# Performance work log

Hardware: AMD Instinct MI355X
Metric: run time of the kernel (lower is better)

## Reference

```python
import jax, jax.numpy as jnp
import numpy as np

N = 8192   # nodes per graph
F = 128    # input feature dim
H = 512    # GAT hidden dim
D = 256    # GAT output dim (== match_size, required by matching broadcast)
MS = 256   # match_size
E = 131072 # edges per graph (one direction)
EPS = 1e-8 # torch cosine_similarity eps


def _xavier(k, shape):
    lim = (6.0 / (shape[0] + shape[-1])) ** 0.5
    return jax.random.uniform(k, shape, jnp.float32, -lim, lim)


def setup_inputs() -> dict:
    key = jax.random.key(0)
    ks = jax.random.split(key, 24)
    return {
        "x_s": jax.random.normal(ks[0], (N, F), jnp.float32),
        "x_t": jax.random.normal(ks[1], (N, F), jnp.float32),
        "edge_index_s": jax.random.randint(ks[2], (2, E), 0, N),
        "edge_index_t": jax.random.randint(ks[3], (2, E), 0, N),
        "label": jax.random.randint(ks[4], (1,), 0, 2),
        # GAT params (2 single-head layers)
        "W_g1": _xavier(ks[5], (F, H)),
        "a1_src": _xavier(ks[6], (H, 1))[:, 0],
        "a1_dst": _xavier(ks[7], (H, 1))[:, 0],
        "W_g2": _xavier(ks[8], (H, D)),
        "a2_src": _xavier(ks[9], (D, 1))[:, 0],
        "a2_dst": _xavier(ks[10], (D, 1))[:, 0],
        # readout_rep
        "W_read": _xavier(ks[11], (D, D)),
        # matching
        "W_match": _xavier(ks[12], (D, MS)),
        # MLP
        "mlp_w1": _xavier(ks[13], (MS * 8, MS * 2)), "mlp_b1": jnp.zeros((MS * 2,), jnp.float32),
        "mlp_w2": _xavier(ks[14], (MS * 2, MS)),     "mlp_b2": jnp.zeros((MS,), jnp.float32),
        "mlp_w3": _xavier(ks[15], (MS, MS // 2)),    "mlp_b3": jnp.zeros((MS // 2,), jnp.float32),
        "mlp_w4": _xavier(ks[16], (MS // 2, 1)),     "mlp_b4": jnp.zeros((1,), jnp.float32),
    }


def _gat_layer(h_in, src, dst, W, a_s, a_d, n):
    h = h_in @ W                                           # [n, d_out]
    logits = (h[src] * a_s).sum(-1) + (h[dst] * a_d).sum(-1)
    e = jax.nn.leaky_relu(logits, 0.2)
    m = jax.ops.segment_max(e, dst, num_segments=n)
    ex = jnp.exp(e - m[dst])
    den = jax.ops.segment_sum(ex, dst, num_segments=n)
    alpha = ex / (den[dst] + 1e-16)
    return jax.ops.segment_sum(alpha[:, None] * h[src], dst, num_segments=n)


def _gat(x, edge_index, W1, a1s, a1d, W2, a2s, a2d):
    n = x.shape[0]
    sl = jnp.arange(n)
    # symmetrize undirected edge list + add self loops (PyG GATConv convention)
    src = jnp.concatenate([edge_index[0], edge_index[1], sl])
    dst = jnp.concatenate([edge_index[1], edge_index[0], sl])
    h = jax.nn.elu(_gat_layer(x, src, dst, W1, a1s, a1d, n))
    return _gat_layer(h, src, dst, W2, a2s, a2d, n)


def _readout(h, W):
    g = jnp.tanh(jnp.mean(h, 0) @ W)                       # [d]
    s = jax.nn.sigmoid(h @ g)                              # [n]
    return (s[:, None] * h).sum(0, keepdims=True)          # [1, d]


def _match(h1, h2, Wm):
    # cosine over feature dim of (h * W) without materializing [N, D, MS]:
    # dot[n,m] = sum_d h1[n,d]*W[d,m]*h2[n,d]*W[d,m] = ((h1*h2) @ W^2)[n,m]
    W2 = Wm * Wm
    dot = (h1 * h2) @ W2
    n1 = jnp.sqrt((h1 * h1) @ W2)
    n2 = jnp.sqrt((h2 * h2) @ W2)
    return dot / jnp.maximum(n1 * n2, EPS)


def _mutual(h1, h2):
    n1 = jnp.linalg.norm(h1, axis=-1)
    n2 = jnp.linalg.norm(h2, axis=-1)
    cos = (h1 @ h2.T) / jnp.maximum(n1[:, None] * n2[None, :], EPS)  # [N, M]
    coe = cos / cos.sum(0)                                 # column-normalize
    return coe @ h2


def _mlp(z, w1, b1, w2, b2, w3, b3, w4, b4):
    z = jax.nn.relu(z @ w1 + b1)
    z = jax.nn.relu(z @ w2 + b2)
    z = jax.nn.relu(z @ w3 + b3)
    return jax.nn.sigmoid(z @ w4 + b4)


def _forward(x_s, x_t, edge_index_s, edge_index_t, label,
             W_g1, a1_src, a1_dst, W_g2, a2_src, a2_dst,
             W_read, W_match,
             mlp_w1, mlp_b1, mlp_w2, mlp_b2, mlp_w3, mlp_b3, mlp_w4, mlp_b4):
    f1 = (x_s - jnp.mean(x_s)) / jnp.std(x_s, ddof=1)
    f2 = (x_t - jnp.mean(x_t)) / jnp.std(x_t, ddof=1)

    h1 = _gat(f1, edge_index_s, W_g1, a1_src, a1_dst, W_g2, a2_src, a2_dst)
    h2 = _gat(f2, edge_index_t, W_g1, a1_src, a1_dst, W_g2, a2_src, a2_dst)

    h1g = _readout(h1, W_read)
    h2g = _readout(h2, W_read)

    h1m = _mutual(h1, h2)
    h2m = _mutual(h2, h1)
    h1mg = _readout(h1m, W_read)
    h2mg = _readout(h2m, W_read)

    miu1 = _match(h1, h1m, W_match); miu2 = _match(h2, h2m, W_match)
    miu1g = _readout(miu1, W_read);  miu2g = _readout(miu2, W_read)
    phi1 = _match(h1, h1mg, W_match); phi2 = _match(h2, h2mg, W_match)
    phi1g = _readout(phi1, W_read);   phi2g = _readout(phi2, W_read)
    psi1 = _match(h1g, h1m, W_match); psi2 = _match(h2g, h2m, W_match)
    psi1g = _readout(psi1, W_read);   psi2g = _readout(psi2, W_read)
    om1 = _match(h1g, h1mg, W_match); om2 = _match(h2g, h2mg, W_match)

    z1 = jnp.concatenate([miu1g, phi1g, psi1g, om1], axis=1).T  # [4*MS, 1]
    z2 = jnp.concatenate([miu2g, phi2g, psi2g, om2], axis=1).T
    z = jnp.concatenate([z1, z2], axis=0).T                     # [1, 8*MS]
    z = _mlp(z, mlp_w1, mlp_b1, mlp_w2, mlp_b2, mlp_w3, mlp_b3, mlp_w4, mlp_b4)
    return z


def reference(x_s, x_t, edge_index_s, edge_index_t, label,
              W_g1, a1_src, a1_dst, W_g2, a2_src, a2_dst,
              W_read, W_match,
              mlp_w1, mlp_b1, mlp_w2, mlp_b2, mlp_w3, mlp_b3, mlp_w4, mlp_b4):
    z = _forward(x_s, x_t, edge_index_s, edge_index_t, label,
                 W_g1, a1_src, a1_dst, W_g2, a2_src, a2_dst, W_read, W_match,
                 mlp_w1, mlp_b1, mlp_w2, mlp_b2, mlp_w3, mlp_b3, mlp_w4, mlp_b4)
    label_exp = jnp.exp(-label.astype(jnp.float32))
    return z, label, label_exp
```

## Files before the change

kernel.cpp:

```cpp
#include <hip/hip_runtime.h>
#include <hip/hip_bf16.h>
#include <math.h>
#include <stddef.h>

#define NN 8192
#define FF 128
#define HH 512
#define DDIM 256
#define EE 131072
#define ET (2*EE + NN)
#define FEPS 1e-8f

typedef float f32x4 __attribute__((ext_vector_type(4)));
typedef __bf16 bf16x8 __attribute__((ext_vector_type(8)));
typedef unsigned short u16;

static __device__ __forceinline__ u16 f2bf(float f) {
  union { float f; unsigned u; } v; v.f = f;
  return (u16)((v.u + 0x7fffu + ((v.u >> 16) & 1u)) >> 16);
}
static __device__ __forceinline__ float bf2f(u16 h) {
  union { unsigned u; float f; } v; v.u = ((unsigned)h) << 16;
  return v.f;
}
static __device__ __forceinline__ f32x4 mfma16(bf16x8 a, bf16x8 b, f32x4 c) {
  return __builtin_amdgcn_mfma_f32_16x16x32_bf16(a, b, c, 0, 0, 0);
}

struct PLF { const float* p[4]; };
struct PLB { const u16* p[6]; int slot[6]; };
struct MB6 { const float* X[6]; const float* Y[6]; int bx[6]; int by[6]; u16* o[6]; };

__global__ void k_reduce2(const float* __restrict__ xa, const float* __restrict__ xb,
                          int n, double* __restrict__ out) {
  const float* x = blockIdx.y ? xb : xa;
  double* o = out + 2 * blockIdx.y;
  __shared__ double s1[256], s2[256];
  double a = 0.0, b = 0.0;
  for (int i = blockIdx.x * blockDim.x + threadIdx.x; i < n; i += gridDim.x * blockDim.x) {
    double v = (double)x[i];
    a += v; b += v * v;
  }
  s1[threadIdx.x] = a; s2[threadIdx.x] = b;
  __syncthreads();
  for (int w = 128; w > 0; w >>= 1) {
    if (threadIdx.x < w) { s1[threadIdx.x] += s1[threadIdx.x + w]; s2[threadIdx.x] += s2[threadIdx.x + w]; }
    __syncthreads();
  }
  if (threadIdx.x == 0) { atomicAdd(&o[0], s1[0]); atomicAdd(&o[1], s2[0]); }
}

__global__ void k_normalize2(const float* __restrict__ xa, const float* __restrict__ xb,
                             u16* __restrict__ ya, u16* __restrict__ yb, int n,
                             const double* __restrict__ s) {
  const float* x = blockIdx.y ? xb : xa;
  u16* y = blockIdx.y ? yb : ya;
  const double* sp = s + 2 * blockIdx.y;
  double mean = sp[0] / (double)n;
  double var = (sp[1] - (double)n * mean * mean) / (double)(n - 1);
  float mu = (float)mean;
  float inv = (float)(1.0 / sqrt(var));
  for (int i = blockIdx.x * blockDim.x + threadIdx.x; i < n; i += gridDim.x * blockDim.x)
    y[i] = f2bf((x[i] - mu) * inv);
}

__global__ void k_hist(const int* __restrict__ ei, int* __restrict__ deg) {
  int t = blockIdx.x * blockDim.x + threadIdx.x;
  if (t >= ET) return;
  int dst = (t < EE) ? ei[EE + t] : ((t < 2*EE) ? ei[t - EE] : (t - 2*EE));
  atomicAdd(&deg[dst], 1);
}

__global__ void k_scan(const int* __restrict__ deg, int* __restrict__ offs, int* __restrict__ cursor) {
  __shared__ int ts[256];
  int tid = threadIdx.x;
  int loc[32];
  int s = 0;
  #pragma unroll
  for (int i = 0; i < 32; ++i) { loc[i] = s; s += deg[tid * 32 + i]; }
  ts[tid] = s;
  __syncthreads();
  for (int off = 1; off < 256; off <<= 1) {
    int v = (tid >= off) ? ts[tid - off] : 0;
    __syncthreads();
// ... 96 lines not shown
  if (as_) {
    float hsum[4] = {0.f, 0.f, 0.f, 0.f}, dsum[4] = {0.f, 0.f, 0.f, 0.f};
    #pragma unroll
    for (int n = 0; n < 8; ++n) {
      int c = n0 + n * 16 + r15;
      float av = as_[c], dv = ad_[c];
      #pragma unroll
      for (int q = 0; q < 4; ++q) { hsum[q] += acc[n][q] * av; dsum[q] += acc[n][q] * dv; }
    }
    #pragma unroll
    for (int q = 0; q < 4; ++q) {
      #pragma unroll
      for (int o = 1; o < 16; o <<= 1) { hsum[q] += __shfl_xor(hsum[q], o); dsum[q] += __shfl_xor(dsum[q], o); }
    }
    if (r15 == 0) {
      #pragma unroll
      for (int q = 0; q < 4; ++q) {
        atomicAdd(&hs[io + q], hsum[q]);
        atomicAdd(&hd[io + q], dsum[q]);
      }
    }
  }
}

__global__ void k_alpha(const int* __restrict__ offs, const int* __restrict__ srcs,
                        const float* __restrict__ hs, const float* __restrict__ hd,
                        float* __restrict__ alpha) {
  int wid = (blockIdx.x * blockDim.x + threadIdx.x) >> 6;
  int lane = threadIdx.x & 63;
  if (wid >= NN) return;
  int b = offs[wid], e = offs[wid + 1];
  float hdn = hd[wid];
  float m = -3.4e38f;
  for (int p = b + lane; p < e; p += 64) {
    float v = hs[srcs[p]] + hdn;
    v = v > 0.f ? v : 0.2f * v;
    alpha[p] = v;
    m = fmaxf(m, v);
  }
  #pragma unroll
  for (int o = 32; o > 0; o >>= 1) m = fmaxf(m, __shfl_xor(m, o));
  float den = 0.f;
  for (int p = b + lane; p < e; p += 64) {
    float ex = expf(alpha[p] - m);
    alpha[p] = ex;
    den += ex;
  }
  #pragma unroll
  for (int o = 32; o > 0; o >>= 1) den += __shfl_xor(den, o);
  float sc = 1.f / (den + 1e-16f);
  for (int p = b + lane; p < e; p += 64) alpha[p] *= sc;
}

__global__ __launch_bounds__(256) void k_agg2(const int* __restrict__ offs, const int* __restrict__ srcs,
                                              const float* __restrict__ alpha, const u16* __restrict__ Hb,
                                              float* __restrict__ outF, u16* __restrict__ outB,
                                              int D, int elu) {
  __shared__ float red[4][512];
  int n = blockIdx.x;
  int b = offs[n], e = offs[n + 1];
  int w = threadIdx.x >> 6, lane = threadIdx.x & 63;
  float acc[8];
  #pragma unroll
  for (int j = 0; j < 8; ++j) acc[j] = 0.f;
  if (D == 512) {
    const u16* base = Hb + lane * 8;
    for (int p = b + w; p < e; p += 4) {
      float a = alpha[p];
      uint4 v = *reinterpret_cast<const uint4*>(base + (size_t)srcs[p] * 512);
      acc[0] += a * bf2f((u16)(v.x & 0xffff)); acc[1] += a * bf2f((u16)(v.x >> 16));
      acc[2] += a * bf2f((u16)(v.y & 0xffff)); acc[3] += a * bf2f((u16)(v.y >> 16));
      acc[4] += a * bf2f((u16)(v.z & 0xffff)); acc[5] += a * bf2f((u16)(v.z >> 16));
      acc[6] += a * bf2f((u16)(v.w & 0xffff)); acc[7] += a * bf2f((u16)(v.w >> 16));
    }
    #pragma unroll
    for (int j = 0; j < 8; ++j) red[w][lane * 8 + j] = acc[j];
  } else {
    const u16* base = Hb + lane * 4;
    for (int p = b + w; p < e; p += 4) {
      float a = alpha[p];
      uint2 v = *reinterpret_cast<const uint2*>(base + (size_t)srcs[p] * 256);
      acc[0] += a * bf2f((u16)(v.x & 0xffff)); acc[1] += a * bf2f((u16)(v.x >> 16));
      acc[2] += a * bf2f((u16)(v.y & 0xffff)); acc[3] += a * bf2f((u16)(v.y >> 16));
    }
    #pragma unroll
    for (int j = 0; j < 4; ++j) red[w][lane * 4 + j] = acc[j];
  }
  __syncthreads();
  for (int dd = threadIdx.x; dd < D; dd += 256) {
    float sres = red[0][dd] + red[1][dd] + red[2][dd] + red[3][dd];
    if (elu) sres = sres > 0.f ? sres : (expf(sres) - 1.f);
    if (outF) outF[(size_t)n * D + dd] = sres;
    outB[(size_t)n * D + dd] = f2bf(sres);
  }
}

__global__ void k_rninv2(const float* __restrict__ h1, const float* __restrict__ h2,
                         float* __restrict__ o1, float* __restrict__ o2) {
  const float* h = blockIdx.y ? h2 : h1;
  float* o = blockIdx.y ? o2 : o1;
  int wid = (blockIdx.x * blockDim.x + threadIdx.x) >> 6;
  int lane = threadIdx.x & 63;
  if (wid >= NN) return;
  float4 v = *reinterpret_cast<const float4*>(h + (size_t)wid * DDIM + lane * 4);
  float a = v.x * v.x + v.y * v.y + v.z * v.z + v.w * v.w;
  #pragma unroll
  for (int o2_ = 32; o2_ > 0; o2_ >>= 1) a += __shfl_xor(a, o2_);
  if (!lane) o[wid] = 1.f / sqrtf(a);
}

__global__ void k_wsum(const float* __restrict__ h1, const float* __restrict__ h2,
                       const float* __restrict__ n1inv, const float* __restrict__ n2inv,
                       float* __restrict__ ut) {
  const float* h = blockIdx.y ? h2 : h1;
  const float* wv = blockIdx.y ? n2inv : n1inv;
  float* o = ut + 256 * blockIdx.y;
  int d = threadIdx.x;
  int r0 = blockIdx.x * 128;
  float acc = 0.f;
  for (int r = 0; r < 128; ++r) acc += wv[r0 + r] * h[(size_t)(r0 + r) * 256 + d];
  atomicAdd(&o[d], acc);
}

__global__ void k_rs(const float* __restrict__ h1, const float* __restrict__ h2,
                     const float* __restrict__ n1inv, const float* __restrict__ n2inv,
                     const float* __restrict__ ut, float* __restrict__ R, float* __restrict__ S) {
  const float* h  = blockIdx.y ? h2 : h1;
  const float* ni = blockIdx.y ? n2inv : n1inv;
  const float* gv = blockIdx.y ? ut : ut + 256;
  float* o = blockIdx.y ? S : R;
  int wid = (blockIdx.x * blockDim.x + threadIdx.x) >> 6;
  int lane = threadIdx.x & 63;
  if (wid >= NN) return;
  float4 v = *reinterpret_cast<const float4*>(h + (size_t)wid * 256 + lane * 4);
  float4 g4 = *reinterpret_cast<const float4*>(gv + lane * 4);
  float a = v.x * g4.x + v.y * g4.y + v.z * g4.z + v.w * g4.w;
  #pragma unroll
  for (int o2_ = 32; o2_ > 0; o2_ >>= 1) a += __shfl_xor(a, o2_);
  if (!lane) o[wid] = ni[wid] * a;
}

__global__ void k_scj(const float* __restrict__ S, const float* __restrict__ R,
                      const float* __restrict__ n1inv, const float* __restrict__ n2inv,
                      float* __restrict__ scj1, float* __restrict__ scj2) {
  int j = blockIdx.x * blockDim.x + threadIdx.x;
  if (j >= NN) return;
  scj1[j] = n2inv[j] / S[j];
  scj2[j] = n1inv[j] / R[j];
}

__global__ __launch_bounds__(256) void k_gemm_M(const u16* __restrict__ A1, const u16* __restrict__ B1,
                                                const u16* __restrict__ A2, const u16* __restrict__ B2,
                                                float* __restrict__ Mf) {
  int mat = blockIdx.z & 1, kch = blockIdx.z >> 1;
  const u16* A = mat ? A2 : A1;
  const u16* Bt = mat ? B2 : B1;
  float* C = Mf + mat * 65536;
  int w = threadIdx.x >> 6, l = threadIdx.x & 63, r15 = l & 15, g = l >> 4;
  int i0 = blockIdx.y * 64 + w * 16;
  int n0 = blockIdx.x * 128;
  f32x4 zero = {0.f, 0.f, 0.f, 0.f};
  f32x4 acc[8];
  #pragma unroll
  for (int n = 0; n < 8; ++n) acc[n] = zero;
  const u16* arow = A + (size_t)(i0 + r15) * NN + g * 8;
  for (int kc = kch * 16; kc < kch * 16 + 16; ++kc) {
    bf16x8 a = *reinterpret_cast<const bf16x8*>(arow + kc * 32);
    #pragma unroll
    for (int n = 0; n < 8; ++n) {
      bf16x8 b = *reinterpret_cast<const bf16x8*>(Bt + (size_t)(n0 + n * 16 + r15) * NN + kc * 32 + g * 8);
      acc[n] = mfma16(a, b, acc[n]);
    }
  }
  int io = i0 + g * 4;
  #pragma unroll
  for (int n = 0; n < 8; ++n) {
    int c = n0 + n * 16 + r15;
    #pragma unroll
    for (int q = 0; q < 4; ++q)
      atomicAdd(&C[(size_t)(io + q) * 256 + c], acc[n][q]);
  }
}

__global__ void k_m2bf(const float* __restrict__ Mf, u16* __restrict__ Mb) {
  size_t o = (size_t)blockIdx.y * 65536 + blockIdx.x * 256 + threadIdx.x;
  Mb[o] = f2bf(Mf[o]);
}

__global__ __launch_bounds__(256) void k_gemm_hm(const u16* __restrict__ A1, const u16* __restrict__ M1,
                                                 const float* __restrict__ s1, float* __restrict__ O1,
                                                 const u16* __restrict__ A2, const u16* __restrict__ M2,
                                                 const float* __restrict__ s2, float* __restrict__ O2) {
  int z = blockIdx.z;
  const u16* A = z ? A2 : A1;
  const u16* Bt = z ? M2 : M1;
  const float* sc = z ? s2 : s1;
  float* O = z ? O2 : O1;
  int w = threadIdx.x >> 6, l = threadIdx.x & 63, r15 = l & 15, g = l >> 4;
  int i0 = blockIdx.y * 64 + w * 16;
  int n0 = blockIdx.x * 128;
  f32x4 zero = {0.f, 0.f, 0.f, 0.f};
  f32x4 acc[8];
  #pragma unroll
  for (int n = 0; n < 8; ++n) acc[n] = zero;
  const u16* arow = A + (size_t)(i0 + r15) * 256 + g * 8;
  #pragma unroll
  for (int kc = 0; kc < 8; ++kc) {
    bf16x8 a = *reinterpret_cast<const bf16x8*>(arow + kc * 32);
    #pragma unroll
    for (int n = 0; n < 8; ++n) {
      bf16x8 b = *reinterpret_cast<const bf16x8*>(Bt + (size_t)(n0 + n * 16 + r15) * 256 + kc * 32 + g * 8);
      acc[n] = mfma16(a, b, acc[n]);
    }
  }
  int io = i0 + g * 4;
  float s4[4];
  #pragma unroll
  for (int q = 0; q < 4; ++q) s4[q] = sc[io + q];
  #pragma unroll
  for (int n = 0; n < 8; ++n) {
    int c = n0 + n * 16 + r15;
    #pragma unroll
    for (int q = 0; q < 4; ++q)
      O[(size_t)(io + q) * 256 + c] = acc[n][q] * s4[q];
  }
}

__global__ __launch_bounds__(256) void k_match_b6(MB6 M, const u16* __restrict__ W2t) {
  int z = blockIdx.z;
  const float* X = M.X[z];
  const float* Y = M.Y[z];
  int bx = M.bx[z], by = M.by[z];
  u16* outb = M.o[z];
  int w = threadIdx.x >> 6, l = threadIdx.x & 63, r15 = l & 15, g = l >> 4;
  int i0 = blockIdx.y * 64 + w * 16;
  int n0 = blockIdx.x * 128;
  f32x4 zero = {0.f, 0.f, 0.f, 0.f};
  f32x4 aU[8], aP[8], aQ[8];
  #pragma unroll
  for (int n = 0; n < 8; ++n) { aU[n] = zero; aP[n] = zero; aQ[n] = zero; }
  int row = i0 + r15;
  const float* xr = X + (size_t)(bx ? 0 : row) * 256;
  const float* yr = Y + (size_t)(by ? 0 : row) * 256;
  #pragma unroll 2
  for (int kc = 0; kc < 8; ++kc) {
    int base = kc * 32 + g * 8;
    float4 x0 = *reinterpret_cast<const float4*>(xr + base);
    float4 x1 = *reinterpret_cast<const float4*>(xr + base + 4);
    float4 y0 = *reinterpret_cast<const float4*>(yr + base);
    float4 y1 = *reinterpret_cast<const float4*>(yr + base + 4);
    bf16x8 fu, fp, fq;
    fu[0] = (__bf16)(x0.x * y0.x); fu[1] = (__bf16)(x0.y * y0.y);
    fu[2] = (__bf16)(x0.z * y0.z); fu[3] = (__bf16)(x0.w * y0.w);
    fu[4] = (__bf16)(x1.x * y1.x); fu[5] = (__bf16)(x1.y * y1.y);
    fu[6] = (__bf16)(x1.z * y1.z); fu[7] = (__bf16)(x1.w * y1.w);
    fp[0] = (__bf16)(x0.x * x0.x); fp[1] = (__bf16)(x0.y * x0.y);
    fp[2] = (__bf16)(x0.z * x0.z); fp[3] = (__bf16)(x0.w * x0.w);
    fp[4] = (__bf16)(x1.x * x1.x); fp[5] = (__bf16)(x1.y * x1.y);
    fp[6] = (__bf16)(x1.z * x1.z); fp[7] = (__bf16)(x1.w * x1.w);
    fq[0] = (__bf16)(y0.x * y0.x); fq[1] = (__bf16)(y0.y * y0.y);
    fq[2] = (__bf16)(y0.z * y0.z); fq[3] = (__bf16)(y0.w * y0.w);
    fq[4] = (__bf16)(y1.x * y1.x); fq[5] = (__bf16)(y1.y * y1.y);
    fq[6] = (__bf16)(y1.z * y1.z); fq[7] = (__bf16)(y1.w * y1.w);
    #pragma unroll
    for (int n = 0; n < 8; ++n) {
      bf16x8 b = *reinterpret_cast<const bf16x8*>(W2t + (size_t)(n0 + n * 16 + r15) * 256 + kc * 32 + g * 8);
      aU[n] = mfma16(fu, b, aU[n]);
      aP[n] = mfma16(fp, b, aP[n]);
      aQ[n] = mfma16(fq, b, aQ[n]);
    }
  }
  int io = i0 + g * 4;
  #pragma unroll
  for (int n = 0; n < 8; ++n) {
    int c = n0 + n * 16 + r15;
    #pragma unroll
    for (int q = 0; q < 4; ++q) {
      float s = sqrtf(aP[n][q]) * sqrtf(aQ[n][q]);
      outb[(size_t)(io + q) * 256 + c] = f2bf(aU[n][q] / fmaxf(s, FEPS));
    }
  }
}

__global__ void k_match_g(const float* __restrict__ X1, const float* __restrict__ Y1,
                          const float* __restrict__ X2, const float* __restrict__ Y2,
                          const float* __restrict__ W2, float* __restrict__ v) {
  __shared__ float u[256], p[256], q[256];
  const float* X = blockIdx.x ? X2 : X1;
  const float* Y = blockIdx.x ? Y2 : Y1;
  float* o = v + (blockIdx.x ? 1792 : 768);
  int t = threadIdx.x;
  float xv = X[t], yv = Y[t];
  u[t] = xv * yv; p[t] = xv * xv; q[t] = yv * yv;
  __syncthreads();
  float a = 0.f, b = 0.f, c = 0.f;
  #pragma unroll 4
  for (int d = 0; d < 256; ++d) {
    float wv = W2[(size_t)d * DDIM + t];
    a += u[d] * wv; b += p[d] * wv; c += q[d] * wv;
  }
  o[t] = a / fmaxf(sqrtf(b) * sqrtf(c), FEPS);
}

__global__ void k_w2(const float* __restrict__ Wm, float* __restrict__ W2, int n) {
  int i = blockIdx.x * blockDim.x + threadIdx.x;
  if (i < n) { float v = Wm[i]; W2[i] = v * v; }
}

__global__ void k_bmu_f(PLF L, float* __restrict__ mu) {
  const float* h = L.p[blockIdx.y];
  int d = threadIdx.x;
  int r0 = blockIdx.x * 128;
  float acc = 0.f;
  for (int r = 0; r < 128; ++r) acc += h[(size_t)(r0 + r) * 256 + d];
  atomicAdd(&mu[blockIdx.y * 256 + d], acc);
}

__global__ void k_bmu_b(PLB L, float* __restrict__ mu) {
  const u16* h = L.p[blockIdx.y];
  int d = threadIdx.x;
  int r0 = blockIdx.x * 128;
  float acc = 0.f;
  for (int r = 0; r < 128; ++r) acc += bf2f(h[(size_t)(r0 + r) * 256 + d]);
  atomicAdd(&mu[blockIdx.y * 256 + d], acc);
}

__global__ void k_bgv(const float* __restrict__ mu, const float* __restrict__ Wr,
                      float* __restrict__ g) {
  __shared__ float ls[256];
  int m = blockIdx.x, t = threadIdx.x;
  ls[t] = mu[m * 256 + t] * (1.f / (float)NN);
  __syncthreads();
  float acc = 0.f;
  #pragma unroll 4
  for (int d = 0; d < 256; ++d) acc += ls[d] * Wr[(size_t)d * 256 + t];
  g[m * 256 + t] = tanhf(acc);
}

__global__ __launch_bounds__(256) void k_bsc_f(PLF L, const float* __restrict__ g,
                                               float* __restrict__ ogbase) {
  __shared__ __align__(16) float gs[256];
  __shared__ float sarr[32];
  int m = blockIdx.y;
  const float* h = L.p[m];
  int t = threadIdx.x, w = t >> 6, l = t & 63;
  gs[t] = g[m * 256 + t];
  __syncthreads();
  int r0 = blockIdx.x * 32;
  float4 gv4 = reinterpret_cast<const float4*>(gs)[l];
  for (int rr = w * 8; rr < w * 8 + 8; ++rr) {
    float4 hv = reinterpret_cast<const float4*>(h + (size_t)(r0 + rr) * 256)[l];
    float dot = hv.x * gv4.x + hv.y * gv4.y + hv.z * gv4.z + hv.w * gv4.w;
    #pragma unroll
    for (int o = 32; o > 0; o >>= 1) dot += __shfl_xor(dot, o);
    if (!l) sarr[rr] = 1.f / (1.f + expf(-dot));
  }
  __syncthreads();
  float acc = 0.f;
  for (int rr = 0; rr < 32; ++rr) acc += sarr[rr] * h[(size_t)(r0 + rr) * 256 + t];
  atomicAdd(&ogbase[m * 256 + t], acc);
}

__global__ __launch_bounds__(256) void k_bsc_b(PLB L, const float* __restrict__ g,
                                               float* __restrict__ v) {
  __shared__ __align__(16) float gs[256];
  __shared__ float sarr[32];
  int m = blockIdx.y;
  const u16* h = L.p[m];
  int t = threadIdx.x, w = t >> 6, l = t & 63;
  gs[t] = g[m * 256 + t];
  __syncthreads();
  int r0 = blockIdx.x * 32;
  float4 gv4 = reinterpret_cast<const float4*>(gs)[l];
  for (int rr = w * 8; rr < w * 8 + 8; ++rr) {
    ushort4 hv = *reinterpret_cast<const ushort4*>(h + (size_t)(r0 + rr) * 256 + l * 4);
    float dot = bf2f(hv.x) * gv4.x + bf2f(hv.y) * gv4.y + bf2f(hv.z) * gv4.z + bf2f(hv.w) * gv4.w;
    #pragma unroll
    for (int o = 32; o > 0; o >>= 1) dot += __shfl_xor(dot, o);
    if (!l) sarr[rr] = 1.f / (1.f + expf(-dot));
  }
  __syncthreads();
  float acc = 0.f;
  for (int rr = 0; rr < 32; ++rr) acc += sarr[rr] * bf2f(h[(size_t)(r0 + rr) * 256 + t]);
  atomicAdd(&v[L.slot[m] + t], acc);
}

__global__ void k_binit(const float* __restrict__ b1, const float* __restrict__ b2,
                        const float* __restrict__ b3, float* __restrict__ l1,
                        float* __restrict__ l2, float* __restrict__ l3) {
  int t = blockIdx.x * 256 + threadIdx.x;
  if (t < 512) l1[t] = b1[t];
  if (t < 256) l2[t] = b2[t];
  if (t < 128) l3[t] = b3[t];
}

__global__ void k_gemv(const float* __restrict__ vin, const float* __restrict__ w,
                       float* __restrict__ out, int K, int M, int Kc, int relu_in) {
  int m = blockIdx.x * 256 + threadIdx.x;
  if (m >= M) return;
  int k0 = blockIdx.y * Kc;
  float acc = 0.f;
  #pragma unroll 4
  for (int k = k0; k < k0 + Kc; ++k) {
    float x = vin[k];
    if (relu_in) x = fmaxf(x, 0.f);
    acc += x * w[(size_t)k * M + m];
  }
  atomicAdd(&out[m], acc);
}

__global__ void k_final(const float* __restrict__ l3, const float* __restrict__ w4,
                        const float* __restrict__ b4, const int* __restrict__ label,
                        float* __restrict__ out) {
  __shared__ float ls[128];
  int t = threadIdx.x;
  ls[t] = fmaxf(l3[t], 0.f) * w4[t];
  __syncthreads();
  for (int w = 64; w > 0; w >>= 1) { if (t < w) ls[t] += ls[t + w]; __syncthreads(); }
  if (t == 0) {
    float z = 1.f / (1.f + expf(-(ls[0] + b4[0])));
    out[0] = z;
    float lb = (float)label[0];
    out[1] = lb;
    out[2] = expf(-lb);
  }
}

extern "C" void kernel_launch(void* const* d_in, const int* in_sizes, int n_in,
                              void* d_out, int out_size, void* d_ws, size_t ws_size,
                              hipStream_t stream) {
  (void)in_sizes; (void)n_in; (void)out_size;
  const float* x_s   = (const float*)d_in[0];
  const float* x_t   = (const float*)d_in[1];
  const int*   ei_s  = (const int*)d_in[2];
  const int*   ei_t  = (const int*)d_in[3];
  const int*   label = (const int*)d_in[4];
  const float* W_g1  = (const float*)d_in[5];
  const float* a1s   = (const float*)d_in[6];
  const float* a1d   = (const float*)d_in[7];
  const float* W_g2  = (const float*)d_in[8];
  const float* a2s   = (const float*)d_in[9];
  const float* a2d   = (const float*)d_in[10];
  const float* W_read  = (const float*)d_in[11];
  const float* W_match = (const float*)d_in[12];
  const float* w1 = (const float*)d_in[13]; const float* b1 = (const float*)d_in[14];
  const float* w2 = (const float*)d_in[15]; const float* b2 = (const float*)d_in[16];
  const float* w3 = (const float*)d_in[17]; const float* b3 = (const float*)d_in[18];
  const float* w4 = (const float*)d_in[19]; const float* b4 = (const float*)d_in[20];
  float* out = (float*)d_out;

  char* base = (char*)d_ws;
  size_t off = 0;
  auto alloc = [&](size_t bytes) -> void* {
    void* pp = base + off;
    off = (off + bytes + 255) & ~(size_t)255;
    return pp;
  };
  double* dsum = (double*)alloc(4 * sizeof(double));
  u16*   hb_bf= (u16*)alloc((size_t)NN * HH * 2);
  u16*   aggb = (u16*)alloc((size_t)NN * HH * 2);
  float* h1   = (float*)alloc((size_t)NN * DDIM * 4);
  float* h2   = (float*)alloc((size_t)NN * DDIM * 4);
  float* h1m  = (float*)alloc((size_t)NN * DDIM * 4);
  float* h2m  = (float*)alloc((size_t)NN * DDIM * 4);
  u16*   f1b  = (u16*)alloc((size_t)NN * FF * 2);
  u16*   f2b  = (u16*)alloc((size_t)NN * FF * 2);
  u16*   h1b  = (u16*)alloc((size_t)NN * DDIM * 2);
  u16*   h2b  = (u16*)alloc((size_t)NN * DDIM * 2);
  u16*   h1t  = (u16*)alloc((size_t)NN * DDIM * 2);
  u16*   h2t  = (u16*)alloc((size_t)NN * DDIM * 2);
  u16*   wh1t = (u16*)alloc((size_t)NN * DDIM * 2);
  u16*   wh2t = (u16*)alloc((size_t)NN * DDIM * 2);
  u16*   mb0  = (u16*)alloc((size_t)NN * DDIM * 2);
  u16*   mb1  = (u16*)alloc((size_t)NN * DDIM * 2);
  u16*   mb2  = (u16*)alloc((size_t)NN * DDIM * 2);
  u16*   mb3  = (u16*)alloc((size_t)NN * DDIM * 2);
  u16*   mb4  = (u16*)alloc((size_t)NN * DDIM * 2);
  u16*   mb5  = (u16*)alloc((size_t)NN * DDIM * 2);
  float* alpha= (float*)alloc((size_t)ET * 4);
  int*   srcs = (int*)alloc((size_t)ET * 4);
  int*   deg  = (int*)alloc(NN * 4);
  int*   curs = (int*)alloc(NN * 4);
  int*   offs = (int*)alloc((NN + 1) * 4);
  float* n1inv= (float*)alloc(NN * 4);
  float* n2inv= (float*)alloc(NN * 4);
  float* Rr   = (float*)alloc(NN * 4);
  float* Ss   = (float*)alloc(NN * 4);
  float* scj1 = (float*)alloc(NN * 4);
  float* scj2 = (float*)alloc(NN * 4);
  float* hsb  = (float*)alloc(NN * 4);
  float* hdb  = (float*)alloc(NN * 4);
  float* W2   = (float*)alloc((size_t)DDIM * DDIM * 4);
  u16*   Wg1t = (u16*)alloc((size_t)HH * FF * 2);
  u16*   Wg2t = (u16*)alloc((size_t)DDIM * HH * 2);
  u16*   W2t  = (u16*)alloc((size_t)DDIM * DDIM * 2);
  u16*   Mb   = (u16*)alloc(2 * 65536 * 2);
  float* mug1 = (float*)alloc(4 * 256 * 4);
  float* ogs  = (float*)alloc(4 * 256 * 4);
  float* mug2 = (float*)alloc(6 * 256 * 4);
  float* v    = (float*)alloc(2048 * 4);
  float* ut   = (float*)alloc(512 * 4);
  float* Mf   = (float*)alloc(2 * 65536 * 4);
  float* g1   = (float*)alloc(4 * 256 * 4);
  float* g2   = (float*)alloc(6 * 256 * 4);
  float* l1o  = (float*)alloc(512 * 4);
  float* l2o  = (float*)alloc(256 * 4);
  float* l3o  = (float*)alloc(128 * 4);
  if (off > ws_size) return;

  float* h1g  = ogs + 0;
  float* h2g  = ogs + 256;
  float* h1mg = ogs + 512;
  float* h2mg = ogs + 768;
  const size_t zr_bytes = (4 * 256 + 4 * 256 + 6 * 256 + 2048 + 512 + 2 * 65536) * 4;

  hipMemsetAsync(dsum, 0, 4 * sizeof(double), stream);
  k_reduce2<<<dim3(1024, 2), 256, 0, stream>>>(x_s, x_t, NN * FF, dsum);
  k_normalize2<<<dim3(1024, 2), 256, 0, stream>>>(x_s, x_t, f1b, f2b, NN * FF, dsum);

  k_tr_bf16<<<dim3(HH / 32, FF / 32), 256, 0, stream>>>(W_g1, Wg1t, FF, HH, 0);
  k_tr_bf16<<<dim3(DDIM / 32, HH / 32), 256, 0, stream>>>(W_g2, Wg2t, HH, DDIM, 0);
  k_tr_bf16<<<dim3(DDIM / 32, DDIM / 32), 256, 0, stream>>>(W_match, W2t, DDIM, DDIM, 1);
  k_w2<<<dim3((DDIM * DDIM + 255) / 256), 256, 0, stream>>>(W_match, W2, DDIM * DDIM);

  auto run_gat = [&](const u16* finb, const int* ei, float* hout, u16* houtb) {
    hipMemsetAsync(deg, 0, NN * 4, stream);
    k_hist<<<dim3((ET + 255) / 256), 256, 0, stream>>>(ei, deg);
    k_scan<<<1, 256, 0, stream>>>(deg, offs, curs);
    k_scatter<<<dim3((ET + 255) / 256), 256, 0, stream>>>(ei, curs, srcs);
    hipMemsetAsync(hsb, 0, 2 * NN * 4, stream);
    k_gemm_bf<<<dim3(HH / 128, NN / 64), 256, 0, stream>>>(finb, Wg1t, hb_bf, FF, HH, a1s, a1d, hsb, hdb);
    k_alpha<<<dim3(NN / 4), 256, 0, stream>>>(offs, srcs, hsb, hdb, alpha);
    k_agg2<<<dim3(NN), 256, 0, stream>>>(offs, srcs, alpha, hb_bf, nullptr, aggb, HH, 1);
    hipMemsetAsync(hsb, 0, 2 * NN * 4, stream);
    k_gemm_bf<<<dim3(DDIM / 128, NN / 64), 256, 0, stream>>>(aggb, Wg2t, hb_bf, HH, DDIM, a2s, a2d, hsb, hdb);
    k_alpha<<<dim3(NN / 4), 256, 0, stream>>>(offs, srcs, hsb, hdb, alpha);
    k_agg2<<<dim3(NN), 256, 0, stream>>>(offs, srcs, alpha, hb_bf, hout, houtb, DDIM, 0);
  };
  run_gat(f1b, ei_s, h1, h1b);
  run_gat(f2b, ei_t, h2, h2b);

  k_rninv2<<<dim3(NN / 4, 2), 256, 0, stream>>>(h1, h2, n1inv, n2inv);
  hipMemsetAsync(mug1, 0, zr_bytes, stream);
  k_wsum<<<dim3(64, 2), 256, 0, stream>>>(h1, h2, n1inv, n2inv, ut);
  k_rs<<<dim3(NN / 4, 2), 256, 0, stream>>>(h1, h2, n1inv, n2inv, ut, Rr, Ss);
  k_scj<<<dim3(NN / 256), 256, 0, stream>>>(Ss, Rr, n1inv, n2inv, scj1, scj2);
  k_tr2w<<<dim3(DDIM / 32, NN / 32, 2), 256, 0, stream>>>(h2, scj1, h2t, wh2t, h1, scj2, h1t, wh1t);
  k_gemm_M<<<dim3(2, 4, 32), 256, 0, stream>>>(wh2t, h2t, wh1t, h1t, Mf);
  k_m2bf<<<dim3(256, 2), 256, 0, stream>>>(Mf, Mb);
  k_gemm_hm<<<dim3(2, 128, 2), 256, 0, stream>>>(h1b, Mb, n1inv, h1m,
                                                 h2b, Mb + 65536, n2inv, h2m);

  PLF g1l; g1l.p[0] = h1; g1l.p[1] = h2; g1l.p[2] = h1m; g1l.p[3] = h2m;
  k_bmu_f<<<dim3(64, 4), 256, 0, stream>>>(g1l, mug1);
  k_bgv<<<dim3(4), 256, 0, stream>>>(mug1, W_read, g1);
  k_bsc_f<<<dim3(256, 4), 256, 0, stream>>>(g1l, g1, ogs);

  MB6 m6;
  m6.X[0] = h1;  m6.Y[0] = h1m;  m6.bx[0] = 0; m6.by[0] = 0; m6.o[0] = mb0;
  m6.X[1] = h1;  m6.Y[1] = h1mg; m6.bx[1] = 0; m6.by[1] = 1; m6.o[1] = mb1;
  m6.X[2] = h1g; m6.Y[2] = h1m;  m6.bx[2] = 1; m6.by[2] = 0; m6.o[2] = mb2;
  m6.X[3] = h2;  m6.Y[3] = h2m;  m6.bx[3] = 0; m6.by[3] = 0; m6.o[3] = mb3;
  m6.X[4] = h2;  m6.Y[4] = h2mg; m6.bx[4] = 0; m6.by[4] = 1; m6.o[4] = mb4;
  m6.X[5] = h2g; m6.Y[5] = h2m;  m6.bx[5] = 1; m6.by[5] = 0; m6.o[5] = mb5;
  k_match_b6<<<dim3(2, NN / 64, 6), 256, 0, stream>>>(m6, W2t);
  k_match_g<<<dim3(2), 256, 0, stream>>>(h1g, h1mg, h2g, h2mg, W2, v);

  PLB g2l;
  g2l.p[0] = mb0; g2l.slot[0] = 0;
  g2l.p[1] = mb1; g2l.slot[1] = 256;
  g2l.p[2] = mb2; g2l.slot[2] = 512;
  g2l.p[3] = mb3; g2l.slot[3] = 1024;
  g2l.p[4] = mb4; g2l.slot[4] = 1280;
  g2l.p[5] = mb5; g2l.slot[5] = 1536;
  k_bmu_b<<<dim3(64, 6), 256, 0, stream>>>(g2l, mug2);
  k_bgv<<<dim3(6), 256, 0, stream>>>(mug2, W_read, g2);
  k_bsc_b<<<dim3(256, 6), 256, 0, stream>>>(g2l, g2, v);

  k_binit<<<dim3(2), 256, 0, stream>>>(b1, b2, b3, l1o, l2o, l3o);
  k_gemv<<<dim3(2, 16), 256, 0, stream>>>(v, w1, l1o, 2048, 512, 128, 0);
  k_gemv<<<dim3(1, 8), 256, 0, stream>>>(l1o, w2, l2o, 512, 256, 64, 1);
  k_gemv<<<dim3(1, 8), 256, 0, stream>>>(l2o, w3, l3o, 256, 128, 32, 1);
  k_final<<<1, 128, 0, stream>>>(l3o, w4, b4, label, out);
}
```

Baseline: 711.7 us.

## Factor matching norms into precomputed reciprocals, bf16 intermediates, per-wave aggregation

The fused matching kernel, which ran three MFMA accumulations (product, x-norm and y-norm) for each of six pairs, is restructured. Squared-norm GEMMs are now computed once per feature matrix into reciprocal-root tables. Broadcast-vector cases fold the global vector into a pre-scaled weight matrix, so each of the six pairs needs only one GEMM. The matched features h1m/h2m are stored in bf16, and the readout kernels now read bf16 instead of fp32. GAT aggregation is changed to one wave per node with no shared-memory reduction. Together these cut MFMA work and memory traffic, at the cost of extra precision loss from storing the reciprocal norms in bf16.

```diff
diff --git a/kernel.cpp b/kernel.cpp
--- a/kernel.cpp
+++ b/kernel.cpp
@@ -27,9 +27,11 @@
   return __builtin_amdgcn_mfma_f32_16x16x32_bf16(a, b, c, 0, 0, 0);
 }
 
-struct PLF { const float* p[4]; };
 struct PLB { const u16* p[6]; int slot[6]; };
-struct MB6 { const float* X[6]; const float* Y[6]; int bx[6]; int by[6]; u16* o[6]; };
+struct MM {
+  const u16* A1[6]; const u16* A2[6]; const u16* B[6];
+  const u16* R1[6]; const u16* R2[6]; const float* Y[6]; u16* o[6];
+};
 
 __global__ void k_reduce2(const float* __restrict__ xa, const float* __restrict__ xb,
                           int n, double* __restrict__ out) {
@@ -232,20 +234,19 @@
   for (int p = b + lane; p < e; p += 64) alpha[p] *= sc;
 }
 
-__global__ __launch_bounds__(256) void k_agg2(const int* __restrict__ offs, const int* __restrict__ srcs,
+__global__ __launch_bounds__(256) void k_agg3(const int* __restrict__ offs, const int* __restrict__ srcs,
                                               const float* __restrict__ alpha, const u16* __restrict__ Hb,
                                               float* __restrict__ outF, u16* __restrict__ outB,
                                               int D, int elu) {
-  __shared__ float red[4][512];
-  int n = blockIdx.x;
+  int wv = threadIdx.x >> 6, lane = threadIdx.x & 63;
+  int n = blockIdx.x * 4 + wv;
   int b = offs[n], e = offs[n + 1];
-  int w = threadIdx.x >> 6, lane = threadIdx.x & 63;
-  float acc[8];
-  #pragma unroll
-  for (int j = 0; j < 8; ++j) acc[j] = 0.f;
   if (D == 512) {
+    float acc[8];
+    #pragma unroll
+    for (int j = 0; j < 8; ++j) acc[j] = 0.f;
     const u16* base = Hb + lane * 8;
-    for (int p = b + w; p < e; p += 4) {
+    for (int p = b; p < e; ++p) {
       float a = alpha[p];
       uint4 v = *reinterpret_cast<const uint4*>(base + (size_t)srcs[p] * 512);
       acc[0] += a * bf2f((u16)(v.x & 0xffff)); acc[1] += a * bf2f((u16)(v.x >> 16));
@@ -253,25 +254,36 @@
       acc[4] += a * bf2f((u16)(v.z & 0xffff)); acc[5] += a * bf2f((u16)(v.z >> 16));
       acc[6] += a * bf2f((u16)(v.w & 0xffff)); acc[7] += a * bf2f((u16)(v.w >> 16));
     }
-    #pragma unroll
-    for (int j = 0; j < 8; ++j) red[w][lane * 8 + j] = acc[j];
+    ushort4 o0, o1;
+    #pragma unroll
+    for (int j = 0; j < 8; ++j)
+      if (elu) acc[j] = acc[j] > 0.f ? acc[j] : (expf(acc[j]) - 1.f);
+    o0.x = f2bf(acc[0]); o0.y = f2bf(acc[1]); o0.z = f2bf(acc[2]); o0.w = f2bf(acc[3]);
+    o1.x = f2bf(acc[4]); o1.y = f2bf(acc[5]); o1.z = f2bf(acc[6]); o1.w = f2bf(acc[7]);
+    u16* ob = outB + (size_t)n * 512 + lane * 8;
+    *reinterpret_cast<ushort4*>(ob) = o0;
+    *reinterpret_cast<ushort4*>(ob + 4) = o1;
   } else {
+    float acc[4];
+    #pragma unroll
+    for (int j = 0; j < 4; ++j) acc[j] = 0.f;
     const u16* base = Hb + lane * 4;
-    for (int p = b + w; p < e; p += 4) {
+    for (int p = b; p < e; ++p) {
       float a = alpha[p];
       uint2 v = *reinterpret_cast<const uint2*>(base + (size_t)srcs[p] * 256);
       acc[0] += a * bf2f((u16)(v.x & 0xffff)); acc[1] += a * bf2f((u16)(v.x >> 16));
       acc[2] += a * bf2f((u16)(v.y & 0xffff)); acc[3] += a * bf2f((u16)(v.y >> 16));
     }
     #pragma unroll
-    for (int j = 0; j < 4; ++j) red[w][lane * 4 + j] = acc[j];
-  }
-  __syncthreads();
-  for (int dd = threadIdx.x; dd < D; dd += 256) {
-    float sres = red[0][dd] + red[1][dd] + red[2][dd] + red[3][dd];
-    if (elu) sres = sres > 0.f ? sres : (expf(sres) - 1.f);
-    if (outF) outF[(size_t)n * D + dd] = sres;
-    outB[(size_t)n * D + dd] = f2bf(sres);
+    for (int j = 0; j < 4; ++j)
+      if (elu) acc[j] = acc[j] > 0.f ? acc[j] : (expf(acc[j]) - 1.f);
+    if (outF) {
+      float4 of = {acc[0], acc[1], acc[2], acc[3]};
+      *reinterpret_cast<float4*>(outF + (size_t)n * 256 + lane * 4) = of;
+    }
+    ushort4 ob;
+    ob.x = f2bf(acc[0]); ob.y = f2bf(acc[1]); ob.z = f2bf(acc[2]); ob.w = f2bf(acc[3]);
+    *reinterpret_cast<ushort4*>(outB + (size_t)n * 256 + lane * 4) = ob;
   }
 }
 
@@ -368,14 +380,14 @@
 }
 
 __global__ __launch_bounds__(256) void k_gemm_hm(const u16* __restrict__ A1, const u16* __restrict__ M1,
-                                                 const float* __restrict__ s1, float* __restrict__ O1,
+                                                 const float* __restrict__ s1, u16* __restrict__ O1,
                                                  const u16* __restrict__ A2, const u16* __restrict__ M2,
-                                                 const float* __restrict__ s2, float* __restrict__ O2) {
+                                                 const float* __restrict__ s2, u16* __restrict__ O2) {
   int z = blockIdx.z;
   const u16* A = z ? A2 : A1;
   const u16* Bt = z ? M2 : M1;
   const float* sc = z ? s2 : s1;
-  float* O = z ? O2 : O1;
+  u16* O = z ? O2 : O1;
   int w = threadIdx.x >> 6, l = threadIdx.x & 63, r15 = l & 15, g = l >> 4;
   int i0 = blockIdx.y * 64 + w * 16;
   int n0 = blockIdx.x * 128;
@@ -402,62 +414,124 @@
     int c = n0 + n * 16 + r15;
     #pragma unroll
     for (int q = 0; q < 4; ++q)
-      O[(size_t)(io + q) * 256 + c] = acc[n][q] * s4[q];
-  }
-}
-
-__global__ __launch_bounds__(256) void k_match_b6(MB6 M, const u16* __restrict__ W2t) {
+      O[(size_t)(io + q) * 256 + c] = f2bf(acc[n][q] * s4[q]);
+  }
+}
+
+__global__ __launch_bounds__(256) void k_matchA(const u16* __restrict__ A0, const u16* __restrict__ A1,
+                                                const u16* __restrict__ A2_, const u16* __restrict__ A3,
+                                                const u16* __restrict__ W2t,
+                                                u16* __restrict__ r0, u16* __restrict__ r1,
+                                                u16* __restrict__ r2, u16* __restrict__ r3) {
   int z = blockIdx.z;
-  const float* X = M.X[z];
+  const u16* A = z == 0 ? A0 : z == 1 ? A1 : z == 2 ? A2_ : A3;
+  u16* outR = z == 0 ? r0 : z == 1 ? r1 : z == 2 ? r2 : r3;
+  int w = threadIdx.x >> 6, l = threadIdx.x & 63, r15 = l & 15, g = l >> 4;
+  int i0 = blockIdx.y * 64 + w * 16;
+  int n0 = blockIdx.x * 128;
+  f32x4 zero = {0.f, 0.f, 0.f, 0.f};
+  f32x4 acc[8];
+  #pragma unroll
+  for (int n = 0; n < 8; ++n) acc[n] = zero;
+  const u16* arow = A + (size_t)(i0 + r15) * 256 + g * 8;
+  #pragma unroll
+  for (int kc = 0; kc < 8; ++kc) {
+    uint4 xv = *reinterpret_cast<const uint4*>(arow + kc * 32);
+    bf16x8 fp;
+    float t;
+    t = bf2f((u16)(xv.x & 0xffff)); fp[0] = (__bf16)(t * t);
+    t = bf2f((u16)(xv.x >> 16));    fp[1] = (__bf16)(t * t);
+    t = bf2f((u16)(xv.y & 0xffff)); fp[2] = (__bf16)(t * t);
+    t = bf2f((u16)(xv.y >> 16));    fp[3] = (__bf16)(t * t);
+    t = bf2f((u16)(xv.z & 0xffff)); fp[4] = (__bf16)(t * t);
+    t = bf2f((u16)(xv.z >> 16));    fp[5] = (__bf16)(t * t);
+    t = bf2f((u16)(xv.w & 0xffff)); fp[6] = (__bf16)(t * t);
+    t = bf2f((u16)(xv.w >> 16));    fp[7] = (__bf16)(t * t);
+    #pragma unroll
+    for (int n = 0; n < 8; ++n) {
+      bf16x8 b = *reinterpret_cast<const bf16x8*>(W2t + (size_t)(n0 + n * 16 + r15) * 256 + kc * 32 + g * 8);
+      acc[n] = mfma16(fp, b, acc[n]);
+    }
+  }
+  int io = i0 + g * 4;
+  #pragma unroll
+  for (int n = 0; n < 8; ++n) {
+    int c = n0 + n * 16 + r15;
+    #pragma unroll
+    for (int q = 0; q < 4; ++q)
+      outR[(size_t)(io + q) * 256 + c] = f2bf(rsqrtf(fmaxf(acc[n][q], 1e-30f)));
+  }
+}
+
+__global__ void k_w2d(const u16* __restrict__ W2t, const float* __restrict__ ogs,
+                      u16* __restrict__ W2d, float* __restrict__ yn) {
+  __shared__ float red[256];
+  int n = blockIdx.x, z = blockIdx.y, k = threadIdx.x;
+  int map = (z == 0) ? 512 : (z == 1) ? 0 : (z == 2) ? 768 : 256;
+  float y = ogs[map + k];
+  float wv = bf2f(W2t[n * 256 + k]);
+  W2d[z * 65536 + n * 256 + k] = f2bf(wv * y);
+  red[k] = wv * y * y;
+  __syncthreads();
+  for (int s = 128; s > 0; s >>= 1) {
+    if (k < s) red[k] += red[k + s];
+    __syncthreads();
+  }
+  if (!k) yn[z * 256 + n] = rsqrtf(fmaxf(red[0], 1e-30f));
+}
+
+__global__ __launch_bounds__(256) void k_matchB(MM M) {
+  int z = blockIdx.z;
+  const u16* A1 = M.A1[z];
+  const u16* A2 = M.A2[z];
+  const u16* Bt = M.B[z];
+  const u16* R1 = M.R1[z];
+  const u16* R2 = M.R2[z];
   const float* Y = M.Y[z];
-  int bx = M.bx[z], by = M.by[z];
   u16* outb = M.o[z];
   int w = threadIdx.x >> 6, l = threadIdx.x & 63, r15 = l & 15, g = l >> 4;
   int i0 = blockIdx.y * 64 + w * 16;
   int n0 = blockIdx.x * 128;
   f32x4 zero = {0.f, 0.f, 0.f, 0.f};
-  f32x4 aU[8], aP[8], aQ[8];
-  #pragma unroll
-  for (int n = 0; n < 8; ++n) { aU[n] = zero; aP[n] = zero; aQ[n] = zero; }
-  int row = i0 + r15;
-  const float* xr = X + (size_t)(bx ? 0 : row) * 256;
-  const float* yr = Y + (size_t)(by ? 0 : row) * 256;
-  #pragma unroll 2
+  f32x4 acc[8];
+  #pragma unroll
+  for (int n = 0; n < 8; ++n) acc[n] = zero;
+  size_t abase = (size_t)(i0 + r15) * 256 + g * 8;
+  #pragma unroll
   for (int kc = 0; kc < 8; ++kc) {
-    int base = kc * 32 + g * 8;
-    float4 x0 = *reinterpret_cast<const float4*>(xr + base);
-    float4 x1 = *reinterpret_cast<const float4*>(xr + base + 4);
-    float4 y0 = *reinterpret_cast<const float4*>(yr + base);
-    float4 y1 = *reinterpret_cast<const float4*>(yr + base + 4);
-    bf16x8 fu, fp, fq;
-    fu[0] = (__bf16)(x0.x * y0.x); fu[1] = (__bf16)(x0.y * y0.y);
-    fu[2] = (__bf16)(x0.z * y0.z); fu[3] = (__bf16)(x0.w * y0.w);
-    fu[4] = (__bf16)(x1.x * y1.x); fu[5] = (__bf16)(x1.y * y1.y);
-    fu[6] = (__bf16)(x1.z * y1.z); fu[7] = (__bf16)(x1.w * y1.w);
-    fp[0] = (__bf16)(x0.x * x0.x); fp[1] = (__bf16)(x0.y * x0.y);
-    fp[2] = (__bf16)(x0.z * x0.z); fp[3] = (__bf16)(x0.w * x0.w);
-    fp[4] = (__bf16)(x1.x * x1.x); fp[5] = (__bf16)(x1.y * x1.y);
-    fp[6] = (__bf16)(x1.z * x1.z); fp[7] = (__bf16)(x1.w * x1.w);
-    fq[0] = (__bf16)(y0.x * y0.x); fq[1] = (__bf16)(y0.y * y0.y);
-    fq[2] = (__bf16)(y0.z * y0.z); fq[3] = (__bf16)(y0.w * y0.w);
-    fq[4] = (__bf16)(y1.x * y1.x); fq[5] = (__bf16)(y1.y * y1.y);
-    fq[6] = (__bf16)(y1.z * y1.z); fq[7] = (__bf16)(y1.w * y1.w);
+    bf16x8 fa;
+    uint4 a = *reinterpret_cast<const uint4*>(A1 + abase + kc * 32);
+    if (A2) {
+      uint4 b2 = *reinterpret_cast<const uint4*>(A2 + abase + kc * 32);
+      fa[0] = (__bf16)(bf2f((u16)(a.x & 0xffff)) * bf2f((u16)(b2.x & 0xffff)));
+      fa[1] = (__bf16)(bf2f((u16)(a.x >> 16))    * bf2f((u16)(b2.x >> 16)));
+      fa[2] = (__bf16)(bf2f((u16)(a.y & 0xffff)) * bf2f((u16)(b2.y & 0xffff)));
+      fa[3] = (__bf16)(bf2f((u16)(a.y >> 16))    * bf2f((u16)(b2.y >> 16)));
+      fa[4] = (__bf16)(bf2f((u16)(a.z & 0xffff)) * bf2f((u16)(b2.z & 0xffff)));
+      fa[5] = (__bf16)(bf2f((u16)(a.z >> 16))    * bf2f((u16)(b2.z >> 16)));
+      fa[6] = (__bf16)(bf2f((u16)(a.w & 0xffff)) * bf2f((u16)(b2.w & 0xffff)));
+      fa[7] = (__bf16)(bf2f((u16)(a.w >> 16))    * bf2f((u16)(b2.w >> 16)));
+    } else {
+      fa = *reinterpret_cast<const bf16x8*>(&a);
+    }
     #pragma unroll
     for (int n = 0; n < 8; ++n) {
-      bf16x8 b = *reinterpret_cast<const bf16x8*>(W2t + (size_t)(n0 + n * 16 + r15) * 256 + kc * 32 + g * 8);
-      aU[n] = mfma16(fu, b, aU[n]);
-      aP[n] = mfma16(fp, b, aP[n]);
-      aQ[n] = mfma16(fq, b, aQ[n]);
+      bf16x8 b = *reinterpret_cast<const bf16x8*>(Bt + (size_t)(n0 + n * 16 + r15) * 256 + kc * 32 + g * 8);
+      acc[n] = mfma16(fa, b, acc[n]);
     }
   }
   int io = i0 + g * 4;
   #pragma unroll
   for (int n = 0; n < 8; ++n) {
     int c = n0 + n * 16 + r15;
+    float yc = Y ? Y[c] : 1.f;
     #pragma unroll
     for (int q = 0; q < 4; ++q) {
-      float s = sqrtf(aP[n][q]) * sqrtf(aQ[n][q]);
-      outb[(size_t)(io + q) * 256 + c] = f2bf(aU[n][q] / fmaxf(s, FEPS));
+      float sc = yc;
+      size_t idx = (size_t)(io + q) * 256 + c;
+      if (R1) sc *= bf2f(R1[idx]);
+      if (R2) sc *= bf2f(R2[idx]);
+      outb[idx] = f2bf(acc[n][q] * sc);
     }
   }
 }
@@ -487,15 +561,6 @@
   if (i < n) { float v = Wm[i]; W2[i] = v * v; }
 }
 
-__global__ void k_bmu_f(PLF L, float* __restrict__ mu) {
-  const float* h = L.p[blockIdx.y];
-  int d = threadIdx.x;
-  int r0 = blockIdx.x * 128;
-  float acc = 0.f;
-  for (int r = 0; r < 128; ++r) acc += h[(size_t)(r0 + r) * 256 + d];
-  atomicAdd(&mu[blockIdx.y * 256 + d], acc);
-}
-
 __global__ void k_bmu_b(PLB L, float* __restrict__ mu) {
   const u16* h = L.p[blockIdx.y];
   int d = threadIdx.x;
@@ -515,30 +580,6 @@
   #pragma unroll 4
   for (int d = 0; d < 256; ++d) acc += ls[d] * Wr[(size_t)d * 256 + t];
   g[m * 256 + t] = tanhf(acc);
-}
-
-__global__ __launch_bounds__(256) void k_bsc_f(PLF L, const float* __restrict__ g,
-                                               float* __restrict__ ogbase) {
-  __shared__ __align__(16) float gs[256];
-  __shared__ float sarr[32];
-  int m = blockIdx.y;
-  const float* h = L.p[m];
-  int t = threadIdx.x, w = t >> 6, l = t & 63;
-  gs[t] = g[m * 256 + t];
-  __syncthreads();
-  int r0 = blockIdx.x * 32;
-  float4 gv4 = reinterpret_cast<const float4*>(gs)[l];
-  for (int rr = w * 8; rr < w * 8 + 8; ++rr) {
-    float4 hv = reinterpret_cast<const float4*>(h + (size_t)(r0 + rr) * 256)[l];
-    float dot = hv.x * gv4.x + hv.y * gv4.y + hv.z * gv4.z + hv.w * gv4.w;
-    #pragma unroll
-    for (int o = 32; o > 0; o >>= 1) dot += __shfl_xor(dot, o);
-    if (!l) sarr[rr] = 1.f / (1.f + expf(-dot));
-  }
-  __syncthreads();
-  float acc = 0.f;
-  for (int rr = 0; rr < 32; ++rr) acc += sarr[rr] * h[(size_t)(r0 + rr) * 256 + t];
-  atomicAdd(&ogbase[m * 256 + t], acc);
 }
 
 __global__ __launch_bounds__(256) void k_bsc_b(PLB L, const float* __restrict__ g,
@@ -641,12 +682,12 @@
   u16*   aggb = (u16*)alloc((size_t)NN * HH * 2);
   float* h1   = (float*)alloc((size_t)NN * DDIM * 4);
   float* h2   = (float*)alloc((size_t)NN * DDIM * 4);
-  float* h1m  = (float*)alloc((size_t)NN * DDIM * 4);
-  float* h2m  = (float*)alloc((size_t)NN * DDIM * 4);
   u16*   f1b  = (u16*)alloc((size_t)NN * FF * 2);
   u16*   f2b  = (u16*)alloc((size_t)NN * FF * 2);
   u16*   h1b  = (u16*)alloc((size_t)NN * DDIM * 2);
   u16*   h2b  = (u16*)alloc((size_t)NN * DDIM * 2);
+  u16*   h1mb = (u16*)alloc((size_t)NN * DDIM * 2);
+  u16*   h2mb = (u16*)alloc((size_t)NN * DDIM * 2);
   u16*   h1t  = (u16*)alloc((size_t)NN * DDIM * 2);
   u16*   h2t  = (u16*)alloc((size_t)NN * DDIM * 2);
   u16*   wh1t = (u16*)alloc((size_t)NN * DDIM * 2);
@@ -657,6 +698,10 @@
   u16*   mb3  = (u16*)alloc((size_t)NN * DDIM * 2);
   u16*   mb4  = (u16*)alloc((size_t)NN * DDIM * 2);
   u16*   mb5  = (u16*)alloc((size_t)NN * DDIM * 2);
+  u16*   rP1  = (u16*)alloc((size_t)NN * DDIM * 2);
+  u16*   rQ1  = (u16*)alloc((size_t)NN * DDIM * 2);
+  u16*   rP2  = (u16*)alloc((size_t)NN * DDIM * 2);
+  u16*   rQ2  = (u16*)alloc((size_t)NN * DDIM * 2);
   float* alpha= (float*)alloc((size_t)ET * 4);
   int*   srcs = (int*)alloc((size_t)ET * 4);
   int*   deg  = (int*)alloc(NN * 4);
@@ -674,6 +719,8 @@
   u16*   Wg1t = (u16*)alloc((size_t)HH * FF * 2);
   u16*   Wg2t = (u16*)alloc((size_t)DDIM * HH * 2);
   u16*   W2t  = (u16*)alloc((size_t)DDIM * DDIM * 2);
+  u16*   W2dB = (u16*)alloc(4 * 65536 * 2);
+  float* ynB  = (float*)alloc(4 * 256 * 4);
   u16*   Mb   = (u16*)alloc(2 * 65536 * 2);
   float* mug1 = (float*)alloc(4 * 256 * 4);
   float* ogs  = (float*)alloc(4 * 256 * 4);
@@ -711,11 +758,11 @@
     hipMemsetAsync(hsb, 0, 2 * NN * 4, stream);
     k_gemm_bf<<<dim3(HH / 128, NN / 64), 256, 0, stream>>>(finb, Wg1t, hb_bf, FF, HH, a1s, a1d, hsb, hdb);
     k_alpha<<<dim3(NN / 4), 256, 0, stream>>>(offs, srcs, hsb, hdb, alpha);
-    k_agg2<<<dim3(NN), 256, 0, stream>>>(offs, srcs, alpha, hb_bf, nullptr, aggb, HH, 1);
+    k_agg3<<<dim3(NN / 4), 256, 0, stream>>>(offs, srcs, alpha, hb_bf, nullptr, aggb, HH, 1);
     hipMemsetAsync(hsb, 0, 2 * NN * 4, stream);
     k_gemm_bf<<<dim3(DDIM / 128, NN / 64), 256, 0, stream>>>(aggb, Wg2t, hb_bf, HH, DDIM, a2s, a2d, hsb, hdb);
     k_alpha<<<dim3(NN / 4), 256, 0, stream>>>(offs, srcs, hsb, hdb, alpha);
-    k_agg2<<<dim3(NN), 256, 0, stream>>>(offs, srcs, alpha, hb_bf, hout, houtb, DDIM, 0);
+    k_agg3<<<dim3(NN / 4), 256, 0, stream>>>(offs, srcs, alpha, hb_bf, hout, houtb, DDIM, 0);
   };
   run_gat(f1b, ei_s, h1, h1b);
   run_gat(f2b, ei_t, h2, h2b);
@@ -728,22 +775,29 @@
   k_tr2w<<<dim3(DDIM / 32, NN / 32, 2), 256, 0, stream>>>(h2, scj1, h2t, wh2t, h1, scj2, h1t, wh1t);
   k_gemm_M<<<dim3(2, 4, 32), 256, 0, stream>>>(wh2t, h2t, wh1t, h1t, Mf);
   k_m2bf<<<dim3(256, 2), 256, 0, stream>>>(Mf, Mb);
-  k_gemm_hm<<<dim3(2, 128, 2), 256, 0, stream>>>(h1b, Mb, n1inv, h1m,
-                                                 h2b, Mb + 65536, n2inv, h2m);
-
-  PLF g1l; g1l.p[0] = h1; g1l.p[1] = h2; g1l.p[2] = h1m; g1l.p[3] = h2m;
-  k_bmu_f<<<dim3(64, 4), 256, 0, stream>>>(g1l, mug1);
+  k_gemm_hm<<<dim3(2, 128, 2), 256, 0, stream>>>(h1b, Mb, n1inv, h1mb,
+                                                 h2b, Mb + 65536, n2inv, h2mb);
+
+  k_matchA<<<dim3(2, 128, 4), 256, 0, stream>>>(h1b, h1mb, h2b, h2mb, W2t, rP1, rQ1, rP2, rQ2);
+
+  PLB g1l;
+  g1l.p[0] = h1b;  g1l.slot[0] = 0;
+  g1l.p[1] = h2b;  g1l.slot[1] = 256;
+  g1l.p[2] = h1mb; g1l.slot[2] = 512;
+  g1l.p[3] = h2mb; g1l.slot[3] = 768;
+  k_bmu_b<<<dim3(64, 4), 256, 0, stream>>>(g1l, mug1);
   k_bgv<<<dim3(4), 256, 0, stream>>>(mug1, W_read, g1);
-  k_bsc_f<<<dim3(256, 4), 256, 0, stream>>>(g1l, g1, ogs);
-
-  MB6 m6;
-  m6.X[0] = h1;  m6.Y[0] = h1m;  m6.bx[0] = 0; m6.by[0] = 0; m6.o[0] = mb0;
-  m6.X[1] = h1;  m6.Y[1] = h1mg; m6.bx[1] = 0; m6.by[1] = 1; m6.o[1] = mb1;
-  m6.X[2] = h1g; m6.Y[2] = h1m;  m6.bx[2] = 1; m6.by[2] = 0; m6.o[2] = mb2;
-  m6.X[3] = h2;  m6.Y[3] = h2m;  m6.bx[3] = 0; m6.by[3] = 0; m6.o[3] = mb3;
-  m6.X[4] = h2;  m6.Y[4] = h2mg; m6.bx[4] = 0; m6.by[4] = 1; m6.o[4] = mb4;
-  m6.X[5] = h2g; m6.Y[5] = h2m;  m6.bx[5] = 1; m6.by[5] = 0; m6.o[5] = mb5;
-  k_match_b6<<<dim3(2, NN / 64, 6), 256, 0, stream>>>(m6, W2t);
+  k_bsc_b<<<dim3(256, 4), 256, 0, stream>>>(g1l, g1, ogs);
+
+  k_w2d<<<dim3(256, 4), 256, 0, stream>>>(W2t, ogs, W2dB, ynB);
+  MM m;
+  m.A1[0] = h1b;  m.A2[0] = h1mb;    m.B[0] = W2t;            m.R1[0] = rP1; m.R2[0] = rQ1;    m.Y[0] = nullptr;   m.o[0] = mb0;
+  m.A1[1] = h1b;  m.A2[1] = nullptr; m.B[1] = W2dB;           m.R1[1] = rP1; m.R2[1] = nullptr; m.Y[1] = ynB;       m.o[1] = mb1;
+  m.A1[2] = h1mb; m.A2[2] = nullptr; m.B[2] = W2dB + 65536;   m.R1[2] = rQ1; m.R2[2] = nullptr; m.Y[2] = ynB + 256; m.o[2] = mb2;
+  m.A1[3] = h2b;  m.A2[3] = h2mb;    m.B[3] = W2t;            m.R1[3] = rP2; m.R2[3] = rQ2;    m.Y[3] = nullptr;   m.o[3] = mb3;
+  m.A1[4] = h2b;  m.A2[4] = nullptr; m.B[4] = W2dB + 2*65536; m.R1[4] = rP2; m.R2[4] = nullptr; m.Y[4] = ynB + 512; m.o[4] = mb4;
+  m.A1[5] = h2mb; m.A2[5] = nullptr; m.B[5] = W2dB + 3*65536; m.R1[5] = rQ2; m.R2[5] = nullptr; m.Y[5] = ynB + 768; m.o[5] = mb5;
+  k_matchB<<<dim3(2, NN / 64, 6), 256, 0, stream>>>(m);
   k_match_g<<<dim3(2), 256, 0, stream>>>(h1g, h1mg, h2g, h2mg, W2, v);
 
   PLB g2l;
```

Result: slower. 746.4 us (+4.9%).
